# Kernel optimization log

Measured on AMD Instinct MI355X. Metric: run time of the kernel, lower is better.

## Reference

```python
import jax, jax.numpy as jnp
import numpy as np

EMBED_DIM = 1024
NUM_HEADS = 16
HEAD_DIM = EMBED_DIM // NUM_HEADS


def setup_inputs() -> dict:
    key = jax.random.key(0)
    ks = jax.random.split(key, 5)
    B, S, D = 2, 2048, EMBED_DIM
    scale = 1.0 / np.sqrt(D)
    x = jax.random.normal(ks[0], (B, S, D), dtype=jnp.float32)
    qkv_w = jax.random.uniform(ks[1], (3 * D, D), dtype=jnp.float32, minval=-scale, maxval=scale)
    qkv_b = jax.random.uniform(ks[2], (3 * D,), dtype=jnp.float32, minval=-scale, maxval=scale)
    out_w = jax.random.uniform(ks[3], (D, D), dtype=jnp.float32, minval=-scale, maxval=scale)
    out_b = jax.random.uniform(ks[4], (D,), dtype=jnp.float32, minval=-scale, maxval=scale)
    return {"x": x, "qkv_w": qkv_w, "qkv_b": qkv_b, "out_w": out_w, "out_b": out_b}


def reference(x, qkv_w, qkv_b, out_w, out_b):
    B, S, D = x.shape
    H, hd = NUM_HEADS, HEAD_DIM
    # QKV projection (torch Linear: y = x @ W^T + b)
    qkv = jnp.einsum('bsd,ed->bse', x, qkv_w) + qkv_b          # [B,S,3D]
    qkv = qkv.reshape(B, S, 3, H, hd)
    q, k, v = (jnp.moveaxis(qkv[:, :, i], 2, 1) for i in range(3))  # each [B,H,S,hd]
    scores = jnp.einsum('bhqd,bhkd->bhqk', q, k) / np.sqrt(hd)  # [B,H,S,S]
    probs = jax.nn.softmax(scores, axis=-1)
    attn = jnp.einsum('bhqk,bhkd->bhqd', probs, v)              # [B,H,S,hd]
    attn = jnp.moveaxis(attn, 1, 2).reshape(B, S, D)
    return jnp.einsum('bsd,ed->bse', attn, out_w) + out_b
```

## Files before the change

kernel.cpp:

```cpp
#include <hip/hip_runtime.h>
#include <stdint.h>

typedef __bf16 bf16;
typedef __attribute__((ext_vector_type(2))) __bf16 bf16x2;
typedef __attribute__((ext_vector_type(4))) __bf16 bf16x4;
typedef __attribute__((ext_vector_type(8))) __bf16 bf16x8;
typedef __attribute__((ext_vector_type(4))) float f32x4;
typedef __attribute__((ext_vector_type(16))) float f32x16;

#define LOG2E_OVER_8 0.18033688011112042f

#if __has_builtin(__builtin_amdgcn_exp2f)
#define EXP2(x) __builtin_amdgcn_exp2f(x)
#else
#define EXP2(x) exp2f(x)
#endif

__device__ __forceinline__ void gl_lds16(const bf16* g, bf16* l) {
  __builtin_amdgcn_global_load_lds(
      (const __attribute__((address_space(1))) void*)g,
      (__attribute__((address_space(3))) void*)l, 16, 0, 0);
}
#define WAIT_VM0_BARRIER() asm volatile("s_waitcnt vmcnt(0)\n\ts_barrier" ::: "memory")

__device__ __forceinline__ uint32_t pack2(float a, float b) {
  union { bf16x2 v; uint32_t u; } z;
  z.v[0] = (bf16)a; z.v[1] = (bf16)b;
  return z.u;
}

__device__ __forceinline__ void pl32swap(uint32_t& a, uint32_t& b) {
  asm("v_permlane32_swap_b32 %0, %1" : "+v"(a), "+v"(b));
}

#define N_X  (4096 * 1024)
#define N_WQ (3072 * 1024)
#define N_WO (1024 * 1024)
__global__ __launch_bounds__(256) void cvt3_kernel(const float* __restrict__ x,
                                                   const float* __restrict__ wq,
                                                   const float* __restrict__ wo,
                                                   bf16* __restrict__ d) {
  int i = (blockIdx.x * 256 + threadIdx.x) * 8;
  const float* s;
  if (i < N_X) s = x + i;
  else if (i < N_X + N_WQ) s = wq + (i - N_X);
  else s = wo + (i - N_X - N_WQ);
  float4 a = *(const float4*)s;
  float4 b = *(const float4*)(s + 4);
  bf16x8 o;
  o[0] = (bf16)a.x; o[1] = (bf16)a.y; o[2] = (bf16)a.z; o[3] = (bf16)a.w;
  o[4] = (bf16)b.x; o[5] = (bf16)b.y; o[6] = (bf16)b.z; o[7] = (bf16)b.w;
  *(bf16x8*)(d + i) = o;
}

template <int EPI>
__global__ __launch_bounds__(256, 3) void gemm_bt(
    const bf16* __restrict__ A, const bf16* __restrict__ Bw,
    const float* __restrict__ bias,
    bf16* __restrict__ qo, bf16* __restrict__ ko, bf16* __restrict__ vTo,
    float* __restrict__ outF) {
  constexpr int MT = EPI ? 64 : 128;
  constexpr int MI = MT / 32;
  constexpr int BK = EPI ? 64 : 32;
  constexpr int NC = BK / 32;
  constexpr int NIT = 1024 / BK;
  constexpr int ASZ = MT * BK;
  constexpr int BSZ = 128 * BK;
  constexpr int RS = 136;
  constexpr int SME0 = 2 * ASZ + 2 * BSZ;
  constexpr int SME = EPI ? SME0 : (SME0 > 128 * RS ? SME0 : 128 * RS);
  __shared__ __attribute__((aligned(16))) bf16 smem[SME];

  int bx, by;
  {
    const int f = blockIdx.x;
    const int xcd = f & 7, idx = f >> 3;
    if constexpr (EPI == 0) { by = xcd * 4 + (idx & 3); bx = idx >> 2; }
    else                    { by = xcd * 8 + (idx & 7); bx = idx >> 3; }
  }

  const int t = threadIdx.x;
  const int L = t & 63;
  const int li = L & 15;
  const int qd = L >> 4;
  const int w = t >> 6;
  const int wm = (w >> 1) * (MT / 2);
  const int wn = (w & 1) * 64;
  const int bm0 = by * MT;
  const int bn0 = bx * 128;
  const int r_st = t >> 2;
  const int c_st = (t & 3) * 8;

  const bf16* Ab = A + (size_t)bm0 * 1024;
  const bf16* Bb = Bw + (size_t)bn0 * 1024;

  auto issue = [&](int k0, int bi) {
    bf16* As_ = smem + bi * ASZ;
    bf16* Bs_ = smem + 2 * ASZ + bi * BSZ;
#pragma unroll
    for (int kc = 0; kc < NC; ++kc) {
      const int kk = k0 + kc * 32;
      gl_lds16(Ab + (size_t)r_st * 1024 + kk + c_st, As_ + kc * MT * 32 + t * 8);
      if constexpr (MT == 128)
        gl_lds16(Ab + (size_t)(r_st + 64) * 1024 + kk + c_st,
                 As_ + kc * MT * 32 + (t + 256) * 8);
      gl_lds16(Bb + (size_t)r_st * 1024 + kk + c_st, Bs_ + kc * 4096 + t * 8);
      gl_lds16(Bb + (size_t)(r_st + 64) * 1024 + kk + c_st,
               Bs_ + kc * 4096 + (t + 256) * 8);
    }
  };

  f32x4 acc[MI][4] = {};
  issue(0, 0);
  for (int it = 0; it < NIT; ++it) {
    WAIT_VM0_BARRIER();
    if (it < NIT - 1) issue((it + 1) * BK, (it + 1) & 1);
    const bf16* Ac = smem + (it & 1) * ASZ;
    const bf16* Bc = smem + 2 * ASZ + (it & 1) * BSZ;
#pragma unroll
    for (int kc = 0; kc < NC; ++kc) {
      const bf16* Ak = Ac + kc * MT * 32;
      const bf16* Bk = Bc + kc * 4096;
      bf16x8 af[MI], bfr[4];
#pragma unroll
      for (int mi = 0; mi < MI; ++mi)
        af[mi] = *(const bf16x8*)(Ak + (wm + mi * 16 + li) * 32 + qd * 8);
#pragma unroll
      for (int ni = 0; ni < 4; ++ni)
        bfr[ni] = *(const bf16x8*)(Bk + (wn + ni * 16 + li) * 32 + qd * 8);
#pragma unroll
      for (int mi = 0; mi < MI; ++mi)
#pragma unroll
        for (int ni = 0; ni < 4; ++ni)
          acc[mi][ni] = __builtin_amdgcn_mfma_f32_16x16x32_bf16(
              af[mi], bfr[ni], acc[mi][ni], 0, 0, 0);
    }
  }

  if constexpr (EPI == 0) {
    const int which = bn0 >> 10;
    __syncthreads();
    bf16* Ct = smem;
    if (which == 2) {
#pragma unroll
      for (int mi = 0; mi < MI; ++mi) {
        const int m_l = wm + mi * 16 + qd * 4;
#pragma unroll
        for (int ni = 0; ni < 4; ++ni) {
          const int n_l = wn + ni * 16 + li;
          const float bi = bias[bn0 + n_l];
          bf16x4 pk;
#pragma unroll
          for (int r = 0; r < 4; ++r) pk[r] = (bf16)(acc[mi][ni][r] + bi);
          *(bf16x4*)(Ct + n_l * RS + m_l) = pk;
        }
      }
    } else {
      const float sc = (which == 0) ? LOG2E_OVER_8 : 1.0f;
#pragma unroll
      for (int mi = 0; mi < MI; ++mi) {
        const int m_l = wm + mi * 16 + qd * 4;
#pragma unroll
        for (int ni = 0; ni < 4; ++ni) {
          const int n_l = wn + ni * 16 + li;
          const float bi = bias[bn0 + n_l];
#pragma unroll
          for (int r = 0; r < 4; ++r)
            Ct[(m_l + r) * RS + n_l] = (bf16)((acc[mi][ni][r] + bi) * sc);
        }
      }
    }
    __syncthreads();
    const int jr = t >> 4;
    const int jc = t & 15;
#pragma unroll
    for (int pass = 0; pass < 8; ++pass) {
      const int row = pass * 16 + jr;
      bf16x8 vv = *(const bf16x8*)(Ct + row * RS + jc * 8);
      if (which == 2) {
        const int n_g = bn0 + row;
        const int hh = (n_g >> 6) & 15, dd = n_g & 63;
        const int bb = bm0 >> 11;
        const int s_b = (bm0 & 2047) + jc * 8;
        *(bf16x8*)(vTo + ((size_t)(bb * 16 + hh) * 64 + dd) * 2048 + s_b) = vv;
      } else {
        const int m_g = bm0 + row;
        const int bb = m_g >> 11, ss = m_g & 2047;
        const int n_g = bn0 + jc * 8;
        const int hh = (n_g >> 6) & 15, dd = n_g & 63;
        bf16* dst = (which == 0 ? qo : ko);
        *(bf16x8*)(dst + ((size_t)(bb * 16 + hh) * 2048 + ss) * 64 + dd) = vv;
      }
    }
  } else {
#pragma unroll
    for (int mi = 0; mi < MI; ++mi) {
      const int m_g = bm0 + wm + mi * 16 + qd * 4;
#pragma unroll
      for (int ni = 0; ni < 4; ++ni) {
        const int n_g = bn0 + wn + ni * 16 + li;
        const float bi = bias[n_g];
#pragma unroll
        for (int r = 0; r < 4; ++r)
          outF[(size_t)(m_g + r) * 1024 + n_g] = acc[mi][ni][r] + bi;
      }
    }
  }
}

__global__ __launch_bounds__(512, 2) void attn_fwd(
    const bf16* __restrict__ Q, const bf16* __restrict__ K,
    const bf16* __restrict__ VT, bf16* __restrict__ AO) {
  __shared__ __attribute__((aligned(16))) bf16 smem[65536];
  const int t = threadIdx.x;
  const int half = t >> 8;
  const int tt = t & 255;
  const int L = t & 63;
  const int m31 = L & 31;
  const int hi = (L >> 5) & 1;
  const int w = (t >> 6) & 3;

  const int lid = blockIdx.x;
  const int bh_ = ((lid & 7) << 2) + (lid >> 6);
  const int qb = (lid >> 3) & 7;
  const int b = bh_ >> 4, h = bh_ & 15;
  const size_t bh = (size_t)(b * 16 + h);

  const bf16* Qp = Q + bh * 2048 * 64;
  const bf16* Kp = K + bh * 2048 * 64 + (size_t)half * 1024 * 64;
  const bf16* Vp = VT + bh * 64 * 2048 + half * 1024;
  const int q0 = qb * 256 + w * 64;

  bf16x8 qf[2][4];
#pragma unroll
  for (int qs = 0; qs < 2; ++qs)
#pragma unroll
    for (int s = 0; s < 4; ++s)
      qf[qs][s] = *(const bf16x8*)(
          Qp + (size_t)(q0 + qs * 32 + m31) * 64 + s * 16 + hi * 8);

  f32x16 acc[2][2] = {};
  float ls[2][2] = {};

  bf16* Kbase = smem + half * 32768;
  bf16* Vbase = Kbase + 16384;

  const int srow = tt >> 3;
  const int scc = (tt & 7) ^ (srow & 7);
  auto issue = [&](int it2, int bi) {
#pragma unroll
    for (int tile = 0; tile < 2; ++tile) {
      const int kt = it2 * 2 + tile;
      const bf16* Kt = Kp + (size_t)kt * 4096;
      const bf16* Vt = Vp + kt * 64;
      bf16* Kd = Kbase + bi * 8192 + tile * 4096;
      bf16* Vd = Vbase + bi * 8192 + tile * 4096;
#pragma unroll
      for (int r = 0; r < 2; ++r) {
        gl_lds16(Kt + (srow + 32 * r) * 64 + scc * 8, Kd + (tt + 256 * r) * 8);
        gl_lds16(Vt + (size_t)(srow + 32 * r) * 2048 + scc * 8, Vd + (tt + 256 * r) * 8);
      }
    }
  };

  const int rlow = m31 & 7;
  union FU { uint32_t u[4]; bf16x8 v; };

  issue(0, 0);
  for (int it2 = 0; it2 < 8; ++it2) {
    WAIT_VM0_BARRIER();
    if (it2 < 7) issue(it2 + 1, (it2 + 1) & 1);
    const bf16* Kc0 = Kbase + (it2 & 1) * 8192;
    const bf16* Vc0 = Vbase + (it2 & 1) * 8192;

    auto QKT = [&](int kt, f32x16* st2) {
      const bf16* Kc = Kc0 + (kt >> 1) * 4096;
      bf16x8 kf[4];
#pragma unroll
      for (int s = 0; s < 4; ++s)
        kf[s] = *(const bf16x8*)(
            Kc + (((kt & 1) * 32 + m31) * 8 + ((2 * s + hi) ^ rlow)) * 8);
      __builtin_amdgcn_s_setprio(1);
#pragma unroll
      for (int qs = 0; qs < 2; ++qs) {
        f32x16 z = {};
#pragma unroll
        for (int s = 0; s < 4; ++s)
          z = __builtin_amdgcn_mfma_f32_32x32x16_bf16(kf[s], qf[qs][s], z, 0, 0, 0);
        st2[qs] = z;
      }
      __builtin_amdgcn_s_setprio(0);
    };

    auto SM = [&](const f32x16& st, int qs, int kt, FU* afp) {
      uint32_t pk[8];
      float lsl = 0.f;
#pragma unroll
      for (int j = 0; j < 8; ++j) {
        float a = EXP2(st[2 * j]);
        float c = EXP2(st[2 * j + 1]);
        lsl += a + c;
        pk[j] = pack2(a, c);
      }
      ls[qs][kt & 1] += lsl;
      pl32swap(pk[0], pk[2]);
      pl32swap(pk[1], pk[3]);
      pl32swap(pk[4], pk[6]);
      pl32swap(pk[5], pk[7]);
      afp[0].u[0] = pk[0]; afp[0].u[1] = pk[1];
      afp[0].u[2] = pk[2]; afp[0].u[3] = pk[3];
      afp[1].u[0] = pk[4]; afp[1].u[1] = pk[5];
      afp[1].u[2] = pk[6]; afp[1].u[3] = pk[7];
    };

    auto PV = [&](int kt, FU A[2][2]) {
      const bf16* Vc = Vc0 + (kt >> 1) * 4096;
      __builtin_amdgcn_s_setprio(1);
#pragma unroll
      for (int dt = 0; dt < 2; ++dt)
#pragma unroll
        for (int u = 0; u < 2; ++u) {
          bf16x8 vf = *(const bf16x8*)(
              Vc + ((dt * 32 + m31) * 8 + (((kt & 1) * 4 + u * 2 + hi) ^ rlow)) * 8);
#pragma unroll
          for (int qs = 0; qs < 2; ++qs)
            acc[dt][qs] = __builtin_amdgcn_mfma_f32_32x32x16_bf16(
                A[qs][u].v, vf, acc[dt][qs], 0, 0, 0);
        }
      __builtin_amdgcn_s_setprio(0);
    };

    f32x16 stc[2], stn[2];
    QKT(0, stc);
#pragma unroll
    for (int kt = 0; kt < 4; ++kt) {
      if (kt < 3) QKT(kt + 1, stn);
      FU A[2][2];
      SM(stc[0], 0, kt, A[0]);
      SM(stc[1], 1, kt, A[1]);
      PV(kt, A);
      stc[0] = stn[0];
      stc[1] = stn[1];
    }
  }

  __syncthreads();
  float* xch = (float*)smem;
  const int slot = w * 64 + L;
  float* rec = xch + slot * 66;
  if (half == 1) {
#pragma unroll
    for (int dt = 0; dt < 2; ++dt)
#pragma unroll
      for (int qs = 0; qs < 2; ++qs)
#pragma unroll
        for (int r = 0; r < 16; ++r)
          rec[dt * 32 + qs * 16 + r] = acc[dt][qs][r];
    rec[64] = ls[0][0] + ls[0][1];
    rec[65] = ls[1][0] + ls[1][1];
  }
  __syncthreads();
  if (half == 0) {
#pragma unroll
    for (int dt = 0; dt < 2; ++dt)
#pragma unroll
      for (int qs = 0; qs < 2; ++qs)
#pragma unroll
        for (int r = 0; r < 16; ++r)
          acc[dt][qs][r] += rec[dt * 32 + qs * 16 + r];

    float inv[2];
#pragma unroll
    for (int qs = 0; qs < 2; ++qs) {
      float l = ls[qs][0] + ls[qs][1] + rec[64 + qs];
      l += __shfl_xor(l, 32);
      inv[qs] = 1.f / l;
    }

#pragma unroll
    for (int qs = 0; qs < 2; ++qs)
#pragma unroll
      for (int r = 0; r < 16; ++r) {
        const int qrow = (r & 3) + 8 * (r >> 2) + 4 * hi;
        const float invq = __shfl(inv[qs], qrow);
        const size_t base =
            ((size_t)b * 2048 + q0 + qs * 32 + qrow) * 1024 + h * 64 + m31;
        AO[base] = (bf16)(acc[0][qs][r] * invq);
        AO[base + 32] = (bf16)(acc[1][qs][r] * invq);
      }
  }
}

extern "C" void kernel_launch(void* const* d_in, const int* in_sizes, int n_in,
                              void* d_out, int out_size, void* d_ws, size_t ws_size,
                              hipStream_t stream) {
  const float* x = (const float*)d_in[0];
  const float* qkvw = (const float*)d_in[1];
  const float* qkvb = (const float*)d_in[2];
  const float* outw = (const float*)d_in[3];
  const float* outb = (const float*)d_in[4];
  float* out = (float*)d_out;

  bf16* xb = (bf16*)d_ws;
  bf16* wq = xb + (size_t)N_X;
  bf16* wo = wq + (size_t)N_WQ;
  bf16* q = wo + (size_t)N_WO;
  bf16* kk = q + (size_t)2 * 16 * 2048 * 64;
  bf16* vT = kk + (size_t)2 * 16 * 2048 * 64;
  bf16* attn = xb;

  cvt3_kernel<<<4096, 256, 0, stream>>>(x, qkvw, outw, xb);

  gemm_bt<0><<<768, 256, 0, stream>>>(xb, wq, qkvb, q, kk, vT, nullptr);
  attn_fwd<<<256, 512, 0, stream>>>(q, kk, vT, attn);
  gemm_bt<1><<<512, 256, 0, stream>>>(attn, wo, outb, nullptr, nullptr, nullptr, out);
}
```

Measured before the change: 172.4 us.

## Hoist K fragment loads per stage and drop QK^T/softmax software pipeline

Loads all K fragments for the four sub-tiles of a stage from LDS up front, behind a sched_barrier. It then runs QK^T, softmax and PV sequentially per sub-tile, with the V fragment loads issued before the softmax. This replaces the previous software pipeline, which computed the next tile's QK^T while doing softmax on the current one. The aim is to batch LDS reads and reduce register pressure from keeping two score tiles live, at the cost of losing MFMA/exp overlap within a wave.

```diff
diff --git a/kernel.cpp b/kernel.cpp
--- a/kernel.cpp
+++ b/kernel.cpp
@@ -266,6 +266,27 @@
   const int rlow = m31 & 7;
   union FU { uint32_t u[4]; bf16x8 v; };
 
+  auto SM = [&](const f32x16& st, int qs, int kt, FU* afp) {
+    uint32_t pk[8];
+    float lsl = 0.f;
+#pragma unroll
+    for (int j = 0; j < 8; ++j) {
+      float a = EXP2(st[2 * j]);
+      float c = EXP2(st[2 * j + 1]);
+      lsl += a + c;
+      pk[j] = pack2(a, c);
+    }
+    ls[qs][kt & 1] += lsl;
+    pl32swap(pk[0], pk[2]);
+    pl32swap(pk[1], pk[3]);
+    pl32swap(pk[4], pk[6]);
+    pl32swap(pk[5], pk[7]);
+    afp[0].u[0] = pk[0]; afp[0].u[1] = pk[1];
+    afp[0].u[2] = pk[2]; afp[0].u[3] = pk[3];
+    afp[1].u[0] = pk[4]; afp[1].u[1] = pk[5];
+    afp[1].u[2] = pk[6]; afp[1].u[3] = pk[7];
+  };
+
   issue(0, 0);
   for (int it2 = 0; it2 < 8; ++it2) {
     WAIT_VM0_BARRIER();
@@ -273,74 +294,55 @@
     const bf16* Kc0 = Kbase + (it2 & 1) * 8192;
     const bf16* Vc0 = Vbase + (it2 & 1) * 8192;
 
-    auto QKT = [&](int kt, f32x16* st2) {
-      const bf16* Kc = Kc0 + (kt >> 1) * 4096;
-      bf16x8 kf[4];
+    bf16x8 kfa[4][4];
+#pragma unroll
+    for (int kt = 0; kt < 4; ++kt)
 #pragma unroll
       for (int s = 0; s < 4; ++s)
-        kf[s] = *(const bf16x8*)(
-            Kc + (((kt & 1) * 32 + m31) * 8 + ((2 * s + hi) ^ rlow)) * 8);
+        kfa[kt][s] = *(const bf16x8*)(
+            Kc0 + (kt >> 1) * 4096 +
+            (((kt & 1) * 32 + m31) * 8 + ((2 * s + hi) ^ rlow)) * 8);
+    __builtin_amdgcn_sched_barrier(0);
+
+#pragma unroll
+    for (int kt = 0; kt < 4; ++kt) {
+      f32x16 st2[2];
       __builtin_amdgcn_s_setprio(1);
 #pragma unroll
       for (int qs = 0; qs < 2; ++qs) {
         f32x16 z = {};
 #pragma unroll
         for (int s = 0; s < 4; ++s)
-          z = __builtin_amdgcn_mfma_f32_32x32x16_bf16(kf[s], qf[qs][s], z, 0, 0, 0);
+          z = __builtin_amdgcn_mfma_f32_32x32x16_bf16(kfa[kt][s], qf[qs][s], z,
+                                                      0, 0, 0);
         st2[qs] = z;
       }
       __builtin_amdgcn_s_setprio(0);
-    };
-
-    auto SM = [&](const f32x16& st, int qs, int kt, FU* afp) {
-      uint32_t pk[8];
-      float lsl = 0.f;
-#pragma unroll
-      for (int j = 0; j < 8; ++j) {
-        float a = EXP2(st[2 * j]);
-        float c = EXP2(st[2 * j + 1]);
-        lsl += a + c;
-        pk[j] = pack2(a, c);
-      }
-      ls[qs][kt & 1] += lsl;
-      pl32swap(pk[0], pk[2]);
-      pl32swap(pk[1], pk[3]);
-      pl32swap(pk[4], pk[6]);
-      pl32swap(pk[5], pk[7]);
-      afp[0].u[0] = pk[0]; afp[0].u[1] = pk[1];
-      afp[0].u[2] = pk[2]; afp[0].u[3] = pk[3];
-      afp[1].u[0] = pk[4]; afp[1].u[1] = pk[5];
-      afp[1].u[2] = pk[6]; afp[1].u[3] = pk[7];
-    };
-
-    auto PV = [&](int kt, FU A[2][2]) {
-      const bf16* Vc = Vc0 + (kt >> 1) * 4096;
+
+      bf16x8 vfa[2][2];
+#pragma unroll
+      for (int dt = 0; dt < 2; ++dt)
+#pragma unroll
+        for (int u = 0; u < 2; ++u)
+          vfa[dt][u] = *(const bf16x8*)(
+              Vc0 + (kt >> 1) * 4096 +
+              ((dt * 32 + m31) * 8 + (((kt & 1) * 4 + u * 2 + hi) ^ rlow)) * 8);
+      __builtin_amdgcn_sched_barrier(0);
+
+      FU A[2][2];
+      SM(st2[0], 0, kt, A[0]);
+      SM(st2[1], 1, kt, A[1]);
+
       __builtin_amdgcn_s_setprio(1);
 #pragma unroll
       for (int dt = 0; dt < 2; ++dt)
 #pragma unroll
-        for (int u = 0; u < 2; ++u) {
-          bf16x8 vf = *(const bf16x8*)(
-              Vc + ((dt * 32 + m31) * 8 + (((kt & 1) * 4 + u * 2 + hi) ^ rlow)) * 8);
+        for (int u = 0; u < 2; ++u)
 #pragma unroll
           for (int qs = 0; qs < 2; ++qs)
             acc[dt][qs] = __builtin_amdgcn_mfma_f32_32x32x16_bf16(
-                A[qs][u].v, vf, acc[dt][qs], 0, 0, 0);
-        }
+                A[qs][u].v, vfa[dt][u], acc[dt][qs], 0, 0, 0);
       __builtin_amdgcn_s_setprio(0);
-    };
-
-    f32x16 stc[2], stn[2];
-    QKT(0, stc);
-#pragma unroll
-    for (int kt = 0; kt < 4; ++kt) {
-      if (kt < 3) QKT(kt + 1, stn);
-      FU A[2][2];
-      SM(stc[0], 0, kt, A[0]);
-      SM(stc[1], 1, kt, A[1]);
-      PV(kt, A);
-      stc[0] = stn[0];
-      stc[1] = stn[1];
     }
   }
 
```

After: 171.0 us. No clear change (-0.8%).

## Split attention keys across four thread quarters per block with 1024 threads

Applied to the files above, without the earlier changes.

The attention kernel now launches 1024 threads per block, split into four groups that each own a quarter of the key range instead of two halves. Each group stages one 64-key tile per iteration, and the two-tile software-pipelined QK^T overlap is replaced by a simpler per-tile loop. Partial accumulators and row sums are combined in a two-level reduction through shared memory, which adds barriers. This deepens key-dimension parallelism per block, at the cost of register budget under launch bounds (1024,1), less in-wave overlap, and a longer reduction tail.

```diff
diff --git a/kernel.cpp b/kernel.cpp
--- a/kernel.cpp
+++ b/kernel.cpp
@@ -208,17 +208,17 @@
   }
 }
 
-__global__ __launch_bounds__(512, 2) void attn_fwd(
+__global__ __launch_bounds__(1024, 1) void attn_fwd(
     const bf16* __restrict__ Q, const bf16* __restrict__ K,
     const bf16* __restrict__ VT, bf16* __restrict__ AO) {
   __shared__ __attribute__((aligned(16))) bf16 smem[65536];
   const int t = threadIdx.x;
-  const int half = t >> 8;
+  const int qtr = t >> 8;
   const int tt = t & 255;
   const int L = t & 63;
   const int m31 = L & 31;
   const int hi = (L >> 5) & 1;
-  const int w = (t >> 6) & 3;
+  const int wq = (t >> 6) & 3;
 
   const int lid = blockIdx.x;
   const int bh_ = ((lid & 7) << 2) + (lid >> 6);
@@ -227,9 +227,9 @@
   const size_t bh = (size_t)(b * 16 + h);
 
   const bf16* Qp = Q + bh * 2048 * 64;
-  const bf16* Kp = K + bh * 2048 * 64 + (size_t)half * 1024 * 64;
-  const bf16* Vp = VT + bh * 64 * 2048 + half * 1024;
-  const int q0 = qb * 256 + w * 64;
+  const bf16* Kp = K + bh * 2048 * 64 + (size_t)qtr * 512 * 64;
+  const bf16* Vp = VT + bh * 64 * 2048 + qtr * 512;
+  const int q0 = qb * 256 + wq * 64;
 
   bf16x8 qf[2][4];
 #pragma unroll
@@ -242,113 +242,98 @@
   f32x16 acc[2][2] = {};
   float ls[2][2] = {};
 
-  bf16* Kbase = smem + half * 32768;
-  bf16* Vbase = Kbase + 16384;
+  bf16* Kbase = smem + qtr * 16384;
+  bf16* Vbase = Kbase + 8192;
 
   const int srow = tt >> 3;
   const int scc = (tt & 7) ^ (srow & 7);
-  auto issue = [&](int it2, int bi) {
-#pragma unroll
-    for (int tile = 0; tile < 2; ++tile) {
-      const int kt = it2 * 2 + tile;
-      const bf16* Kt = Kp + (size_t)kt * 4096;
-      const bf16* Vt = Vp + kt * 64;
-      bf16* Kd = Kbase + bi * 8192 + tile * 4096;
-      bf16* Vd = Vbase + bi * 8192 + tile * 4096;
-#pragma unroll
-      for (int r = 0; r < 2; ++r) {
-        gl_lds16(Kt + (srow + 32 * r) * 64 + scc * 8, Kd + (tt + 256 * r) * 8);
-        gl_lds16(Vt + (size_t)(srow + 32 * r) * 2048 + scc * 8, Vd + (tt + 256 * r) * 8);
-      }
+  auto issue = [&](int itK, int bi) {
+    const bf16* Kt = Kp + (size_t)itK * 4096;
+    const bf16* Vt = Vp + itK * 64;
+    bf16* Kd = Kbase + bi * 4096;
+    bf16* Vd = Vbase + bi * 4096;
+#pragma unroll
+    for (int r = 0; r < 2; ++r) {
+      gl_lds16(Kt + (srow + 32 * r) * 64 + scc * 8, Kd + (tt + 256 * r) * 8);
+      gl_lds16(Vt + (size_t)(srow + 32 * r) * 2048 + scc * 8, Vd + (tt + 256 * r) * 8);
     }
   };
 
   const int rlow = m31 & 7;
   union FU { uint32_t u[4]; bf16x8 v; };
 
+  auto SM = [&](const f32x16& st, int qs, int kt, FU* afp) {
+    uint32_t pk[8];
+    float lsl = 0.f;
+#pragma unroll
+    for (int j = 0; j < 8; ++j) {
+      float a = EXP2(st[2 * j]);
+      float c = EXP2(st[2 * j + 1]);
+      lsl += a + c;
+      pk[j] = pack2(a, c);
+    }
+    ls[qs][kt] += lsl;
+    pl32swap(pk[0], pk[2]);
+    pl32swap(pk[1], pk[3]);
+    pl32swap(pk[4], pk[6]);
+    pl32swap(pk[5], pk[7]);
+    afp[0].u[0] = pk[0]; afp[0].u[1] = pk[1];
+    afp[0].u[2] = pk[2]; afp[0].u[3] = pk[3];
+    afp[1].u[0] = pk[4]; afp[1].u[1] = pk[5];
+    afp[1].u[2] = pk[6]; afp[1].u[3] = pk[7];
+  };
+
   issue(0, 0);
-  for (int it2 = 0; it2 < 8; ++it2) {
+  for (int itK = 0; itK < 8; ++itK) {
     WAIT_VM0_BARRIER();
-    if (it2 < 7) issue(it2 + 1, (it2 + 1) & 1);
-    const bf16* Kc0 = Kbase + (it2 & 1) * 8192;
-    const bf16* Vc0 = Vbase + (it2 & 1) * 8192;
-
-    auto QKT = [&](int kt, f32x16* st2) {
-      const bf16* Kc = Kc0 + (kt >> 1) * 4096;
+    if (itK < 7) issue(itK + 1, (itK + 1) & 1);
+    const bf16* Kc = Kbase + (itK & 1) * 4096;
+    const bf16* Vc = Vbase + (itK & 1) * 4096;
+
+#pragma unroll
+    for (int kt = 0; kt < 2; ++kt) {
       bf16x8 kf[4];
 #pragma unroll
       for (int s = 0; s < 4; ++s)
         kf[s] = *(const bf16x8*)(
-            Kc + (((kt & 1) * 32 + m31) * 8 + ((2 * s + hi) ^ rlow)) * 8);
-      __builtin_amdgcn_s_setprio(1);
+            Kc + ((kt * 32 + m31) * 8 + ((2 * s + hi) ^ rlow)) * 8);
+
+      FU A[2][2];
 #pragma unroll
       for (int qs = 0; qs < 2; ++qs) {
         f32x16 z = {};
+        __builtin_amdgcn_s_setprio(1);
 #pragma unroll
         for (int s = 0; s < 4; ++s)
           z = __builtin_amdgcn_mfma_f32_32x32x16_bf16(kf[s], qf[qs][s], z, 0, 0, 0);
-        st2[qs] = z;
-      }
-      __builtin_amdgcn_s_setprio(0);
-    };
-
-    auto SM = [&](const f32x16& st, int qs, int kt, FU* afp) {
-      uint32_t pk[8];
-      float lsl = 0.f;
-#pragma unroll
-      for (int j = 0; j < 8; ++j) {
-        float a = EXP2(st[2 * j]);
-        float c = EXP2(st[2 * j + 1]);
-        lsl += a + c;
-        pk[j] = pack2(a, c);
-      }
-      ls[qs][kt & 1] += lsl;
-      pl32swap(pk[0], pk[2]);
-      pl32swap(pk[1], pk[3]);
-      pl32swap(pk[4], pk[6]);
-      pl32swap(pk[5], pk[7]);
-      afp[0].u[0] = pk[0]; afp[0].u[1] = pk[1];
-      afp[0].u[2] = pk[2]; afp[0].u[3] = pk[3];
-      afp[1].u[0] = pk[4]; afp[1].u[1] = pk[5];
-      afp[1].u[2] = pk[6]; afp[1].u[3] = pk[7];
-    };
-
-    auto PV = [&](int kt, FU A[2][2]) {
-      const bf16* Vc = Vc0 + (kt >> 1) * 4096;
+        __builtin_amdgcn_s_setprio(0);
+        SM(z, qs, kt, A[qs]);
+      }
+
       __builtin_amdgcn_s_setprio(1);
 #pragma unroll
       for (int dt = 0; dt < 2; ++dt)
 #pragma unroll
         for (int u = 0; u < 2; ++u) {
           bf16x8 vf = *(const bf16x8*)(
-              Vc + ((dt * 32 + m31) * 8 + (((kt & 1) * 4 + u * 2 + hi) ^ rlow)) * 8);
+              Vc + ((dt * 32 + m31) * 8 + ((kt * 4 + u * 2 + hi) ^ rlow)) * 8);
 #pragma unroll
           for (int qs = 0; qs < 2; ++qs)
             acc[dt][qs] = __builtin_amdgcn_mfma_f32_32x32x16_bf16(
                 A[qs][u].v, vf, acc[dt][qs], 0, 0, 0);
         }
       __builtin_amdgcn_s_setprio(0);
-    };
-
-    f32x16 stc[2], stn[2];
-    QKT(0, stc);
-#pragma unroll
-    for (int kt = 0; kt < 4; ++kt) {
-      if (kt < 3) QKT(kt + 1, stn);
-      FU A[2][2];
-      SM(stc[0], 0, kt, A[0]);
-      SM(stc[1], 1, kt, A[1]);
-      PV(kt, A);
-      stc[0] = stn[0];
-      stc[1] = stn[1];
     }
   }
 
-  __syncthreads();
+  float lsq[2];
+#pragma unroll
+  for (int qs = 0; qs < 2; ++qs) lsq[qs] = ls[qs][0] + ls[qs][1];
+
   float* xch = (float*)smem;
-  const int slot = w * 64 + L;
-  float* rec = xch + slot * 66;
-  if (half == 1) {
+  float* rec = xch + (wq * 64 + L) * 66;
+
+  auto put = [&]() {
 #pragma unroll
     for (int dt = 0; dt < 2; ++dt)
 #pragma unroll
@@ -356,11 +341,10 @@
 #pragma unroll
         for (int r = 0; r < 16; ++r)
           rec[dt * 32 + qs * 16 + r] = acc[dt][qs][r];
-    rec[64] = ls[0][0] + ls[0][1];
-    rec[65] = ls[1][0] + ls[1][1];
-  }
-  __syncthreads();
-  if (half == 0) {
+    rec[64] = lsq[0];
+    rec[65] = lsq[1];
+  };
+  auto get_add = [&]() {
 #pragma unroll
     for (int dt = 0; dt < 2; ++dt)
 #pragma unroll
@@ -368,11 +352,26 @@
 #pragma unroll
         for (int r = 0; r < 16; ++r)
           acc[dt][qs][r] += rec[dt * 32 + qs * 16 + r];
+    lsq[0] += rec[64];
+    lsq[1] += rec[65];
+  };
+
+  __syncthreads();
+  if (qtr == 1) put();
+  __syncthreads();
+  if (qtr == 0) get_add();
+  __syncthreads();
+  if (qtr == 3) put();
+  __syncthreads();
+  if (qtr == 2) { get_add(); put(); }
+  __syncthreads();
+  if (qtr == 0) {
+    get_add();
 
     float inv[2];
 #pragma unroll
     for (int qs = 0; qs < 2; ++qs) {
-      float l = ls[qs][0] + ls[qs][1] + rec[64 + qs];
+      float l = lsq[qs];
       l += __shfl_xor(l, 32);
       inv[qs] = 1.f / l;
     }
@@ -412,6 +411,6 @@
   cvt3_kernel<<<4096, 256, 0, stream>>>(x, qkvw, outw, xb);
 
   gemm_bt<0><<<768, 256, 0, stream>>>(xb, wq, qkvb, q, kk, vT, nullptr);
-  attn_fwd<<<256, 512, 0, stream>>>(q, kk, vT, attn);
+  attn_fwd<<<256, 1024, 0, stream>>>(q, kk, vT, attn);
   gemm_bt<1><<<512, 256, 0, stream>>>(attn, wo, outb, nullptr, nullptr, nullptr, out);
 }
```

Measured after the change: 406.0 us. 136% more time.
